# Kernel tuning notes

Hardware: AMD Instinct MI355X
Metric: run time of the kernel (lower is better)

The kernel has to match this reference:

```python
import jax, jax.numpy as jnp
import numpy as np

STRIDE = 16
SCALES = (0.5, 1.0, 2.0)
RATIOS = (0.5, 1.0, 2.0)
IOU_THR = 0.7
CONF_THR = 0.5
KEEP_PRE = 6000
KEEP_POST = 300


def _default_boxes(fh, fw):
    # anchors centered at origin: size = stride*scale, w/h set by aspect ratio
    s = STRIDE * jnp.asarray(SCALES, jnp.float32)                    # [S]
    r = jnp.asarray(RATIOS, jnp.float32)                             # [R]
    w = (s[None, :] * jnp.sqrt(1.0 / r)[:, None]).reshape(-1)        # [A]
    h = (s[None, :] * jnp.sqrt(r)[:, None]).reshape(-1)              # [A]
    anchors = jnp.stack([-w / 2, -h / 2, w / 2, h / 2], axis=-1)     # [A,4]
    sx = jnp.arange(fw, dtype=jnp.float32) * STRIDE
    sy = jnp.arange(fh, dtype=jnp.float32) * STRIDE
    gx, gy = jnp.meshgrid(sx, sy)                                    # [fh,fw]
    shifts = jnp.stack([gx, gy, gx, gy], axis=-1)                    # [fh,fw,4]
    return (shifts[:, :, None, :] + anchors[None, None, :, :]).reshape(-1, 4)


def _apply_regs(deltas, boxes):
    # deltas: [bs,N,4] (dx,dy,dw,dh); boxes: [N,4] xyxy default boxes
    w = boxes[:, 2] - boxes[:, 0]
    h = boxes[:, 3] - boxes[:, 1]
    cx = boxes[:, 0] + 0.5 * w
    cy = boxes[:, 1] + 0.5 * h
    pcx = deltas[..., 0] * w + cx
    pcy = deltas[..., 1] * h + cy
    pw = jnp.exp(deltas[..., 2]) * w
    ph = jnp.exp(deltas[..., 3]) * h
    return jnp.stack([pcx - 0.5 * pw, pcy - 0.5 * ph,
                      pcx + 0.5 * pw, pcy + 0.5 * ph], axis=-1)


def _clip(boxes, img_h, img_w):
    lim = jnp.asarray([img_w, img_h, img_w, img_h], jnp.float32)
    return jnp.clip(boxes, 0.0, lim)


def _pairwise_iou(b):
    area = jnp.maximum(b[:, 2] - b[:, 0], 0.0) * jnp.maximum(b[:, 3] - b[:, 1], 0.0)
    lt = jnp.maximum(b[:, None, :2], b[None, :, :2])
    rb = jnp.minimum(b[:, None, 2:], b[None, :, 2:])
    wh = jnp.maximum(rb - lt, 0.0)
    inter = wh[..., 0] * wh[..., 1]
    union = area[:, None] + area[None, :] - inter
    return inter / jnp.maximum(union, 1e-9)


def _nms_keep(boxes, thr):
    # boxes are pre-sorted by descending score -> greedy NMS == row sweep
    n = boxes.shape[0]
    iou = _pairwise_iou(jax.lax.stop_gradient(boxes))  # [n,n]
    idx = jnp.arange(n)
    def body(i, keep):
        sup = (iou[i] > thr) & (idx > i)
        return keep & jnp.where(keep[i], ~sup, True)
    return jax.lax.fori_loop(0, n, body, jnp.ones(n, dtype=bool))


def _detect_one(boxes, scores):
    order = jnp.argsort(-scores)
    props = boxes[order][:KEEP_PRE]          # [P,4]
    sc = scores[order][:KEEP_PRE]            # [P]
    keep = _nms_keep(props, IOU_THR)
    pos = jnp.cumsum(keep) - 1               # compacted position of kept boxes
    valid = keep & (pos < KEEP_POST)
    dst = jnp.where(valid, pos, KEEP_POST)   # out-of-range -> dropped by scatter
    out_b = jnp.zeros((KEEP_POST, 4), props.dtype).at[dst].set(props, mode='drop')
    out_s = jnp.zeros((KEEP_POST,), sc.dtype).at[dst].set(sc, mode='drop')
    # confidence filter: zero out rows below threshold (fixed-shape analog of list)
    return out_b * (out_s > CONF_THR).astype(props.dtype)[:, None]


def reference(preds, regs, img_h, img_w):
    bs, fh, fw, na = preds.shape
    db = _default_boxes(fh, fw)                          # [fh*fw*A, 4]
    scores = jax.nn.sigmoid(preds).reshape(bs, -1)       # [bs, N]
    boxes = _apply_regs(regs.reshape(bs, -1, 4), db)     # [bs, N, 4]
    boxes = _clip(boxes, img_h, img_w)
    outs = [_detect_one(boxes[i], scores[i]) for i in range(bs)]
    return jnp.stack(outs)                               # [bs, KEEP_POST, 4]


def setup_inputs() -> dict:
    key = jax.random.key(0)
    k1, k2 = jax.random.split(key)
    preds = jax.random.normal(k1, (4, 37, 62, 9), jnp.float32)
    regs = jax.random.normal(k2, (4, 37, 62, 9, 4), jnp.float32)
    return {"preds": preds, "regs": regs, "img_h": 600, "img_w": 1000}
```

## Files before the change

kernel.cpp:

```cpp
#include <hip/hip_runtime.h>
#include <stdint.h>

typedef unsigned long long u64;
typedef unsigned int u32;

#define FH 37
#define FW 62
#define NA 9
#define NPRED 20646
#define BS 4
#define KEEP_PRE 6000
#define KEEP_POST 300
#define NBINS 4096
#define SELCAP 3072
#define SLOTN 6144
#define FB_BASE 4608
#define NFB 640
#define NCHUNK 21
#define FSLOTS 32
#define FSUB 64
#define NFINE 2048

#define L_HIST   0u
#define L_SUF    16384u
#define L_RG1    32768u
#define L_RG2    81920u
#define L_FBCUR  106496u
#define L_PERM   109056u
#define L_KBOX   121344u
#define L_KAREA  126208u
#define L_WSUM   127424u
#define L_WPOS   127488u
#define L_SCAL   127552u
#define L_AW     127616u
#define L_MROW   127744u
#define LDS_TOTAL 128256u

__device__ __forceinline__ u32 mapbits(float p) {
  u32 u = __float_as_uint(p);
  return (u & 0x80000000u) ? ~u : (u | 0x80000000u);
}
__device__ __forceinline__ bool iou_sup(float kx1, float ky1, float kx2, float ky2,
                                        float ka, float cx1, float cy1,
                                        float cx2, float cy2, float ca) {
  float wx = fmaxf(fminf(kx2, cx2) - fmaxf(kx1, cx1), 0.f);
  float wy = fmaxf(fminf(ky2, cy2) - fmaxf(ky1, cy1), 0.f);
  float inter = wx * wy;
  float un = ka + ca - inter;
  return inter > 0.7f * fmaxf(un, 1e-9f);
}
__device__ __forceinline__ float4 decode_box(u32 n, float4 d, float W, float H) {
  int a = (int)(n % NA);
  int cell = (int)(n / NA);
  int x = cell % FW;
  int y = cell / FW;
  int si = a % 3, ri = a / 3;
  float s = (si==0) ? 8.f : ((si==1) ? 16.f : 32.f);
  float r = (ri==0) ? 0.5f : ((ri==1) ? 1.0f : 2.0f);
  float aw = s * sqrtf(1.0f / r);
  float ah = s * sqrtf(r);
  float gx = (float)x * 16.f, gy = (float)y * 16.f;
  float x1d = gx - 0.5f*aw, x2d = gx + 0.5f*aw;
  float y1d = gy - 0.5f*ah, y2d = gy + 0.5f*ah;
  float w = x2d - x1d, h = y2d - y1d;
  float cx = x1d + 0.5f*w, cy = y1d + 0.5f*h;
  float pcx = d.x*w + cx, pcy = d.y*h + cy;
  float pw = expf(d.z)*w, ph = expf(d.w)*h;
  float bx1 = fminf(fmaxf(pcx - 0.5f*pw, 0.f), W);
  float by1 = fminf(fmaxf(pcy - 0.5f*ph, 0.f), H);
  float bx2 = fminf(fmaxf(pcx + 0.5f*pw, 0.f), W);
  float by2 = fminf(fmaxf(pcy + 0.5f*ph, 0.f), H);
  return make_float4(bx1, by1, bx2, by2);
}

__global__ void __launch_bounds__(1024) detect_kernel(
    const float* __restrict__ preds, const float4* __restrict__ regs4,
    const int* __restrict__ ih, const int* __restrict__ iw,
    float4* __restrict__ out)
{
  __shared__ __align__(16) char smem[LDS_TOTAL];
  u32*    histL  = (u32*)(smem + L_HIST);
  u32*    sufL   = (u32*)(smem + L_SUF);
  u32*    repl   = (u32*)(smem + L_RG1);
  u64*    slots  = (u64*)(smem + L_RG1);
  float4* cboxL  = (float4*)(smem + L_RG1);
  u32*    fineH  = (u32*)(smem + L_RG2);
  u32*    fineS  = (u32*)(smem + L_RG2 + 8192);
  u32*    fineC  = (u32*)(smem + L_RG2 + 16384);
  float*  careaL = (float*)(smem + L_RG2);
  u32*    fbCur  = (u32*)(smem + L_FBCUR);
  u32*    perm   = (u32*)(smem + L_PERM);
  float4* kbox   = (float4*)(smem + L_KBOX);
  float*  karea  = (float*)(smem + L_KAREA);
  u32*    wsum   = (u32*)(smem + L_WSUM);
  u32*    wpos   = (u32*)(smem + L_WPOS);
  u32*    scal   = (u32*)(smem + L_SCAL);
  u64*    aw     = (u64*)(smem + L_AW);
  u64*    mrow   = (u64*)(smem + L_MROW);

  const int b = blockIdx.x;
  const int t = threadIdx.x;
  const int lane = t & 63;
  const int wv = t >> 6;
  const float* pb = preds + b*NPRED;
  const float4* rb = regs4 + b*NPRED;
  const float W = (float)(*iw), H = (float)(*ih);
  float4* ob = out + b*KEEP_POST;
  const float4 zero = make_float4(0.f, 0.f, 0.f, 0.f);

  #pragma unroll
  for (int q = 0; q < 4; ++q) histL[q*1024 + t] = 0;
  #pragma unroll
  for (int q = 0; q < 12; ++q) repl[q*1024 + t] = 0;
  if (t == 0) scal[2] = 0;
  __syncthreads();

  {
    u32* repA = ((wv & 3) == 0) ? histL : (repl + ((wv & 3) - 1) * 4096);
    u32 mypos = 0;
    #pragma unroll 4
    for (int c = 0; c < NCHUNK; ++c) {
      int n = c*1024 + t;
      bool valid = (n < NPRED);
      float p = valid ? pb[n] : -1.0f;
      u64 bm = __ballot(valid && (p > 0.0f));
      mypos += (u32)__popcll(bm);
      if (valid) atomicAdd(&repA[mapbits(p) >> 20], 1u);
    }
    if (lane == 0) wpos[wv] = mypos;
  }
  __syncthreads();

  {
    u32* r2 = repl + 4096; u32* r3 = repl + 8192;
    u32 h0 = histL[4*t+0] + repl[4*t+0] + r2[4*t+0] + r3[4*t+0];
    u32 h1 = histL[4*t+1] + repl[4*t+1] + r2[4*t+1] + r3[4*t+1];
    u32 h2 = histL[4*t+2] + repl[4*t+2] + r2[4*t+2] + r3[4*t+2];
    u32 h3 = histL[4*t+3] + repl[4*t+3] + r2[4*t+3] + r3[4*t+3];
    histL[4*t+0]=h0; histL[4*t+1]=h1; histL[4*t+2]=h2; histL[4*t+3]=h3;
    u32 s = h0 + h1 + h2 + h3;
    u32 sf = s;
    #pragma unroll
    for (int off = 1; off < 64; off <<= 1) {
      u32 o = __shfl_down(sf, off, 64);
      if (lane + off < 64) sf += o;
    }
    if (lane == 0) wsum[wv] = sf;
    __syncthreads();
    u32 hi = 0;
    for (int w2 = wv + 1; w2 < 16; ++w2) hi += wsum[w2];
    u32 St = hi + (sf - s);
    u32 s3 = St, s2 = s3 + h3, s1 = s2 + h2, s0 = s1 + h1;
    sufL[4*t+0]=s0; sufL[4*t+1]=s1; sufL[4*t+2]=s2; sufL[4*t+3]=s3;
    if (t == 0) {
      u32 np = 0;
      #pragma unroll
      for (int w2 = 0; w2 < 16; ++w2) np += wpos[w2];
      scal[3] = np;
    }
  }
  __syncthreads();

  #pragma unroll 1
  for (int tr = 0; tr < 2; ++tr) {
    const u32 winStart = (u32)tr * SELCAP;
    const u32 winEnd = winStart + SELCAP;
    const int rowLimit = (KEEP_PRE - (int)winStart < (int)SELCAP)
                           ? (KEEP_PRE - (int)winStart) : (int)SELCAP;

    if (t == 0) { scal[0] = 0xFFFFFFFFu; scal[1] = 0u; }
    __syncthreads();
    #pragma unroll
    for (int q = 0; q < 4; ++q) {
      int v = 4*t + q;
      u32 hv = histL[v], sv = sufL[v];
      if (hv && sv < winEnd && sv + hv > winStart) {
        atomicMin(&scal[0], (u32)v);
        atomicMax(&scal[1], (u32)v);
      }
    }
    __syncthreads();
    const u32 binLo = scal[0], binHi = scal[1];
    u32 cBase = binLo;
    if (binHi - binLo >= FSLOTS) cBase = binHi - (FSLOTS - 1);
    const u32 S_top = sufL[binHi];
    const u32 S_cb = (cBase > 0) ? sufL[cBase-1] : 0;
    const u32 rebWinEnd = winEnd - S_top;

    #pragma unroll
    for (int q = 0; q < 2; ++q) fineH[q*1024 + t] = 0;
    #pragma unroll
    for (int q = 0; q < 6; ++q) slots[q*1024 + t] = 0ull;
    if (t < NFB) {
      u32 v = binLo + (u32)t;
      fbCur[t] = (v < cBase) ? (FB_BASE + (sufL[v] - S_cb)) : (u32)SLOTN;
    }
    __syncthreads();

    #pragma unroll 4
    for (int c = 0; c < NCHUNK; ++c) {
      int n = c*1024 + t;
      if (n < NPRED) {
        u32 m = mapbits(pb[n]);
        u32 cb = m >> 20;
        if (cb >= cBase && cb <= binHi)
          atomicAdd(&fineH[((cb - cBase) << 6) | ((m >> 14) & 0x3F)], 1u);
      }
    }
    __syncthreads();

    {
      u32 f0 = fineH[2*t], f1 = fineH[2*t+1];
      u32 s = f0 + f1;
      u32 sf = s;
      #pragma unroll
      for (int off = 1; off < 64; off <<= 1) {
        u32 o = __shfl_down(sf, off, 64);
        if (lane + off < 64) sf += o;
      }
      if (lane == 0) wsum[wv] = sf;
      __syncthreads();
      u32 hi = 0;
      for (int w2 = wv + 1; w2 < 16; ++w2) hi += wsum[w2];
      u32 St = hi + (sf - s);
      u32 sA = St + f1, sB = St;
      fineS[2*t] = sA; fineS[2*t+1] = sB;
      fineC[2*t] = sA; fineC[2*t+1] = sB;
    }
    __syncthreads();

    #pragma unroll 4
    for (int c = 0; c < NCHUNK; ++c) {
      int n = c*1024 + t;
      if (n < NPRED) {
        u32 m = mapbits(pb[n]);
        u32 cb = m >> 20;
        u64 key = ((u64)m << 32) | (u32)(~(u32)n);
        if (cb >= cBase && cb <= binHi) {
          u32 F = ((cb - cBase) << 6) | ((m >> 14) & 0x3F);
          if (fineS[F] < rebWinEnd) {
            u32 pos = atomicAdd(&fineC[F], 1u);
            if (pos < FB_BASE) slots[pos] = key;
          }
        } else if (cb >= binLo && cb < cBase) {
          u32 fo = cb - binLo;
          if (fo < NFB) {
            u32 pos = atomicAdd(&fbCur[fo], 1u);
            if (pos < SLOTN) slots[pos] = key;
          }
        }
      }
    }
    __syncthreads();

    #pragma unroll
    for (int q = 0; q < 6; ++q) {
      int i = q*1024 + t;
      u64 k = slots[i];
      if (k != 0) {
        u32 m = (u32)(k >> 32);
        u32 cb = m >> 20;
        u32 rank;
        if (cb >= cBase) {
          u32 F = ((cb - cBase) << 6) | ((m >> 14) & 0x3F);
          u32 base = fineS[F];
          u32 end = base + fineH[F]; if (end > FB_BASE) end = FB_BASE;
          u32 c2 = 0;
          for (u32 j = base; j < end; ++j) c2 += (slots[j] > k) ? 1u : 0u;
          rank = S_top + fineS[F] + c2;
        } else {
          u32 base = FB_BASE + (sufL[cb] - S_cb);
          u32 end = base + histL[cb]; if (end > SLOTN) end = SLOTN;
          u32 c2 = 0;
          for (u32 j = base; j < end; ++j) c2 += (slots[j] > k) ? 1u : 0u;
          rank = sufL[cb] + c2;
        }
        int local = (int)rank - (int)winStart;
        if (local >= 0 && local < rowLimit) perm[local] = ~(u32)k;
      }
    }
    __syncthreads();

    for (int r = t; r < rowLimit; r += 1024) {
      u32 idx = perm[r];
      float4 bx = decode_box(idx, rb[idx], W, H);
      cboxL[r] = bx;
      careaL[r] = (bx.z - bx.x) * (bx.w - bx.y);
    }
    __syncthreads();

    {
      const int npos = (int)scal[3];
      const int nblk = (rowLimit + 63) >> 6;
      for (int blk = 0; blk < nblk; ++blk) {
        int cnt = (int)scal[2];
        if (cnt >= KEEP_POST) break;
        const int base = blk * 64;
        const int ci = base + lane;
        const bool valid = (ci < rowLimit);
        float4 cur = cboxL[valid ? ci : 0];
        float carea = careaL[valid ? ci : 0];

        int dead = 0;
        for (int k = wv; k < cnt; k += 16) {
          float4 kb = kbox[k];
          dead |= (int)iou_sup(kb.x, kb.y, kb.z, kb.w, karea[k],
                               cur.x, cur.y, cur.z, cur.w, carea);
        }
        aw[wv] = __ballot(dead);

        #pragma unroll
        for (int q = 0; q < 4; ++q) {
          int j = wv*4 + q;
          int jr = base + j; if (jr >= rowLimit) jr = 0;
          float4 bj = cboxL[jr];
          float ja = careaL[jr];
          bool s = iou_sup(bj.x, bj.y, bj.z, bj.w, ja,
                           cur.x, cur.y, cur.z, cur.w, carea);
          u64 bm = __ballot(s);
          if (lane == 0) mrow[j] = bm;
        }
        __syncthreads();

        if (wv == 0) {
          u64 deadAll = 0;
          #pragma unroll
          for (int k = 0; k < 16; ++k) deadAll |= aw[k];
          int rem = rowLimit - base;
          u64 vm = (rem >= 64) ? ~0ull : ((1ull << rem) - 1ull);
          u64 A = vm & ~deadAll;
          int c2 = cnt;
          while (A && c2 < KEEP_POST) {
            int j = (int)__builtin_ctzll(A);
            A &= A - 1;
            A &= ~mrow[j];
            if (lane == 0) {
              float4 bj = cboxL[base + j];
              kbox[c2] = bj;
              karea[c2] = careaL[base + j];
              ob[c2] = ((int)(winStart + (u32)(base + j)) < npos) ? bj : zero;
            }
            ++c2;
          }
          if (lane == 0) scal[2] = (u32)c2;
        }
        __syncthreads();
      }
    }
    if ((int)scal[2] >= KEEP_POST) break;
  }

  for (int k2 = (int)scal[2] + t; k2 < KEEP_POST; k2 += 1024) ob[k2] = zero;
}

extern "C" void kernel_launch(void* const* d_in, const int* in_sizes, int n_in,
                              void* d_out, int out_size, void* d_ws, size_t ws_size,
                              hipStream_t stream) {
  const float* preds  = (const float*)d_in[0];
  const float4* regs4 = (const float4*)d_in[1];
  const int* ih       = (const int*)d_in[2];
  const int* iw       = (const int*)d_in[3];
  (void)d_ws; (void)ws_size; (void)in_sizes; (void)n_in; (void)out_size;

  detect_kernel<<<dim3(BS), 1024, 0, stream>>>(
      preds, regs4, ih, iw, (float4*)d_out);
}
```

Before: 172.0 us.

## Skip intra-block IoU for dead candidates and use readlane in greedy NMS sweep

The NMS block loop now adds a barrier after the kept-box suppression ballot, so every wave builds the alive mask itself. A block whose candidates are all suppressed is skipped, and intra-block IoU rows are computed only for surviving candidates. The serial greedy scan keeps the mask rows in registers and reads them with readlane instead of LDS loads. The change also double-buffers the aw array, unrolls the rank-counting loop by 4, and unrolls the wave-sum prefix loops, at the cost of one extra barrier per block.

```diff
diff --git a/kernel.cpp b/kernel.cpp
--- a/kernel.cpp
+++ b/kernel.cpp
@@ -19,7 +19,6 @@
 #define NCHUNK 21
 #define FSLOTS 32
 #define FSUB 64
-#define NFINE 2048
 
 #define L_HIST   0u
 #define L_SUF    16384u
@@ -33,12 +32,17 @@
 #define L_WPOS   127488u
 #define L_SCAL   127552u
 #define L_AW     127616u
-#define L_MROW   127744u
-#define LDS_TOTAL 128256u
+#define L_MROW   127872u
+#define LDS_TOTAL 128384u
 
 __device__ __forceinline__ u32 mapbits(float p) {
   u32 u = __float_as_uint(p);
   return (u & 0x80000000u) ? ~u : (u | 0x80000000u);
+}
+__device__ __forceinline__ u64 readlane64(u64 v, int srcLane) {
+  u32 lo = __builtin_amdgcn_readlane((u32)v, srcLane);
+  u32 hi = __builtin_amdgcn_readlane((u32)(v >> 32), srcLane);
+  return ((u64)hi << 32) | lo;
 }
 __device__ __forceinline__ bool iou_sup(float kx1, float ky1, float kx2, float ky2,
                                         float ka, float cx1, float cy1,
@@ -148,7 +152,8 @@
     if (lane == 0) wsum[wv] = sf;
     __syncthreads();
     u32 hi = 0;
-    for (int w2 = wv + 1; w2 < 16; ++w2) hi += wsum[w2];
+    #pragma unroll
+    for (int w2 = 0; w2 < 16; ++w2) hi += (w2 > wv) ? wsum[w2] : 0u;
     u32 St = hi + (sf - s);
     u32 s3 = St, s2 = s3 + h3, s1 = s2 + h2, s0 = s1 + h1;
     sufL[4*t+0]=s0; sufL[4*t+1]=s1; sufL[4*t+2]=s2; sufL[4*t+3]=s3;
@@ -221,7 +226,8 @@
       if (lane == 0) wsum[wv] = sf;
       __syncthreads();
       u32 hi = 0;
-      for (int w2 = wv + 1; w2 < 16; ++w2) hi += wsum[w2];
+      #pragma unroll
+      for (int w2 = 0; w2 < 16; ++w2) hi += (w2 > wv) ? wsum[w2] : 0u;
       u32 St = hi + (sf - s);
       u32 sA = St + f1, sB = St;
       fineS[2*t] = sA; fineS[2*t+1] = sB;
@@ -260,22 +266,26 @@
       if (k != 0) {
         u32 m = (u32)(k >> 32);
         u32 cb = m >> 20;
-        u32 rank;
+        u32 base, end, rbase;
         if (cb >= cBase) {
           u32 F = ((cb - cBase) << 6) | ((m >> 14) & 0x3F);
-          u32 base = fineS[F];
-          u32 end = base + fineH[F]; if (end > FB_BASE) end = FB_BASE;
-          u32 c2 = 0;
-          for (u32 j = base; j < end; ++j) c2 += (slots[j] > k) ? 1u : 0u;
-          rank = S_top + fineS[F] + c2;
+          base = fineS[F];
+          end = base + fineH[F]; if (end > FB_BASE) end = FB_BASE;
+          rbase = S_top + fineS[F];
         } else {
-          u32 base = FB_BASE + (sufL[cb] - S_cb);
-          u32 end = base + histL[cb]; if (end > SLOTN) end = SLOTN;
-          u32 c2 = 0;
-          for (u32 j = base; j < end; ++j) c2 += (slots[j] > k) ? 1u : 0u;
-          rank = sufL[cb] + c2;
-        }
-        int local = (int)rank - (int)winStart;
+          base = FB_BASE + (sufL[cb] - S_cb);
+          end = base + histL[cb]; if (end > SLOTN) end = SLOTN;
+          rbase = sufL[cb];
+        }
+        u32 c2 = 0;
+        for (u32 j = base; j < end; j += 4) {
+          u64 s0 = slots[j];
+          u64 s1 = (j+1 < end) ? slots[j+1] : 0ull;
+          u64 s2 = (j+2 < end) ? slots[j+2] : 0ull;
+          u64 s3 = (j+3 < end) ? slots[j+3] : 0ull;
+          c2 += (u32)(s0 > k) + (u32)(s1 > k) + (u32)(s2 > k) + (u32)(s3 > k);
+        }
+        int local = (int)(rbase + c2) - (int)winStart;
         if (local >= 0 && local < rowLimit) perm[local] = ~(u32)k;
       }
     }
@@ -302,38 +312,47 @@
         float carea = careaL[valid ? ci : 0];
 
         int dead = 0;
+        #pragma unroll 2
         for (int k = wv; k < cnt; k += 16) {
           float4 kb = kbox[k];
           dead |= (int)iou_sup(kb.x, kb.y, kb.z, kb.w, karea[k],
                                cur.x, cur.y, cur.z, cur.w, carea);
         }
-        aw[wv] = __ballot(dead);
+        u64* awb = aw + ((blk & 1) << 4);
+        awb[wv] = __ballot(dead);
+        __syncthreads();
+
+        u64 deadAll = 0;
+        #pragma unroll
+        for (int k = 0; k < 16; ++k) deadAll |= awb[k];
+        int rem = rowLimit - base;
+        u64 vm = (rem >= 64) ? ~0ull : ((1ull << rem) - 1ull);
+        u64 A = vm & ~deadAll;
+        if (A == 0) continue;
 
         #pragma unroll
         for (int q = 0; q < 4; ++q) {
           int j = wv*4 + q;
-          int jr = base + j; if (jr >= rowLimit) jr = 0;
-          float4 bj = cboxL[jr];
-          float ja = careaL[jr];
-          bool s = iou_sup(bj.x, bj.y, bj.z, bj.w, ja,
-                           cur.x, cur.y, cur.z, cur.w, carea);
-          u64 bm = __ballot(s);
-          if (lane == 0) mrow[j] = bm;
+          if ((A >> j) & 1ull) {
+            float4 bj = cboxL[base + j];
+            float ja = careaL[base + j];
+            bool s = iou_sup(bj.x, bj.y, bj.z, bj.w, ja,
+                             cur.x, cur.y, cur.z, cur.w, carea);
+            u64 bm = __ballot(s);
+            if (lane == 0) mrow[j] = bm;
+          } else if (lane == 0) {
+            mrow[j] = 0ull;
+          }
         }
         __syncthreads();
 
         if (wv == 0) {
-          u64 deadAll = 0;
-          #pragma unroll
-          for (int k = 0; k < 16; ++k) deadAll |= aw[k];
-          int rem = rowLimit - base;
-          u64 vm = (rem >= 64) ? ~0ull : ((1ull << rem) - 1ull);
-          u64 A = vm & ~deadAll;
+          u64 mreg = mrow[lane];
           int c2 = cnt;
           while (A && c2 < KEEP_POST) {
             int j = (int)__builtin_ctzll(A);
             A &= A - 1;
-            A &= ~mrow[j];
+            A &= ~readlane64(mreg, j);
             if (lane == 0) {
               float4 bj = cboxL[base + j];
               kbox[c2] = bj;
@@ -347,6 +366,7 @@
         __syncthreads();
       }
     }
+    __syncthreads();
     if ((int)scal[2] >= KEEP_POST) break;
   }
 
```

Measured after the change: 174.2 us. Within noise of the previous version (+1.3%).
